# Optimization experiments

Hardware: AMD Instinct MI355X
Metric: run time of the kernel (lower is better)

Reference implementation:

```python
import jax, jax.numpy as jnp
import numpy as np

NUM_HEADS = 16
D_MODEL = 1024
B, T = 2, 2048


def setup_inputs() -> dict:
    key = jax.random.key(0)
    ks = jax.random.split(key, 5)
    s = 1.0 / np.sqrt(D_MODEL)
    return {
        "x": jax.random.normal(ks[0], (B, T, D_MODEL), dtype=jnp.float32),
        "Wq": jax.random.normal(ks[1], (D_MODEL, D_MODEL), dtype=jnp.float32) * s,
        "Wk": jax.random.normal(ks[2], (D_MODEL, D_MODEL), dtype=jnp.float32) * s,
        "Wv": jax.random.normal(ks[3], (D_MODEL, D_MODEL), dtype=jnp.float32) * s,
        "Wo": jax.random.normal(ks[4], (D_MODEL, D_MODEL), dtype=jnp.float32) * s,
    }


def reference(x, Wq, Wk, Wv, Wo):
    # x: [B, T, D]; W*: [D, D] (torch nn.Linear weight layout, y = x @ W.T)
    b, t, d = x.shape
    h = NUM_HEADS
    hd = d // h

    def split_heads(y):
        # [B, T, D] -> [B, H, T, hd]
        return y.reshape(b, t, h, hd).transpose(0, 2, 1, 3)

    q = split_heads(x @ Wq.T)
    k = split_heads(x @ Wk.T)
    v = split_heads(x @ Wv.T)

    # scale uses last dim AFTER head split: 1/sqrt(head_dim)
    scores = jnp.einsum("bhqd,bhkd->bhqk", q, k) / jnp.sqrt(jnp.asarray(hd, x.dtype))
    causal = jnp.tril(jnp.ones((t, t), dtype=bool))  # [T, T]
    scores = jnp.where(causal[None, None], scores, -jnp.inf)
    attn = jax.nn.softmax(scores, axis=-1)  # [B, H, T, T]

    out = jnp.einsum("bhqk,bhkd->bhqd", attn, v)  # [B, H, T, hd]
    out = out.transpose(0, 2, 1, 3).reshape(b, t, d)  # concat heads
    return out @ Wo.T
```

## Files before the change

kernel.cpp:

```cpp
#include <hip/hip_runtime.h>
#include <hip/hip_bf16.h>

#define T_SEQ 2048
#define DM    1024
#define MTOT  4096

typedef short v8s __attribute__((ext_vector_type(8)));
typedef short v4s __attribute__((ext_vector_type(4)));
typedef float v4f __attribute__((ext_vector_type(4)));

__device__ __forceinline__ unsigned short f2bf(float f) {
  union { float f; unsigned int u; } x; x.f = f;
  return (unsigned short)((x.u + (((x.u >> 16) & 1u) + 0x7fffu)) >> 16);
}

__device__ __forceinline__ unsigned int pk2(float a, float b) {
  unsigned int ua = __float_as_uint(a) + 0x8000u;
  unsigned int ub = __float_as_uint(b) + 0x8000u;
  return __builtin_amdgcn_perm(ub, ua, 0x07060302u);
}

__device__ __forceinline__ v8s pack8bf(v4f a, v4f b) {
  union { v8s s; unsigned int u[4]; } o;
  o.u[0] = pk2(a[0], a[1]);
  o.u[1] = pk2(a[2], a[3]);
  o.u[2] = pk2(b[0], b[1]);
  o.u[3] = pk2(b[2], b[3]);
  return o.s;
}

__device__ __forceinline__ float fast_exp2(float x) {
#if __has_builtin(__builtin_amdgcn_exp2f)
  return __builtin_amdgcn_exp2f(x);
#else
  return exp2f(x);
#endif
}

__device__ __forceinline__ void gload16(const void* g, void* lds) {
  __builtin_amdgcn_global_load_lds(
      (const __attribute__((address_space(1))) unsigned int*)g,
      (__attribute__((address_space(3))) unsigned int*)lds, 16, 0, 0);
}

__global__ __launch_bounds__(256) void convert_all(
    const float* __restrict__ x,
    const float* __restrict__ Wq, const float* __restrict__ Wk,
    const float* __restrict__ Wv, const float* __restrict__ Wo,
    unsigned short* __restrict__ xb, unsigned short* __restrict__ wb)
{
  int i = blockIdx.x * 256 + threadIdx.x;
  const float4* src;
  ushort4* dst;
  int idx;
  if (i < (1 << 20)) {
    src = (const float4*)x; dst = (ushort4*)xb; idx = i;
  } else {
    int j = i - (1 << 20);
    int wsel = j >> 18;
    idx = j & ((1 << 18) - 1);
    const float* s = (wsel == 0) ? Wq : (wsel == 1) ? Wk : (wsel == 2) ? Wv : Wo;
    src = (const float4*)s;
    dst = (ushort4*)(wb + (size_t)wsel * DM * DM);
  }
  float4 v = src[idx];
  ushort4 o = { f2bf(v.x), f2bf(v.y), f2bf(v.z), f2bf(v.w) };
  dst[idx] = o;
}

__global__ __launch_bounds__(256) void qkv_fused4(
    const unsigned short* __restrict__ xb,
    const unsigned short* __restrict__ wb,
    unsigned short* __restrict__ Qw, unsigned short* __restrict__ Kw,
    unsigned short* __restrict__ Vtw)
{
  __shared__ unsigned short smem[2][20480];

  const int tid  = threadIdx.x;
  const int wv   = tid >> 6, l = tid & 63;
  const int lrow = l & 15, lq = l >> 4;
  const int wm = wv >> 1;
  const int wn = wv & 1;
  const int srow = l >> 3, sslot = l & 7;
  const int swz  = sslot ^ (srow & 7);
  const int m0 = blockIdx.x * 128, n0 = blockIdx.y * 64;

  v4f acc[3][4][2];
#pragma unroll
  for (int z = 0; z < 3; ++z)
#pragma unroll
    for (int mt = 0; mt < 4; ++mt)
#pragma unroll
      for (int nt = 0; nt < 2; ++nt) acc[z][mt][nt] = (v4f){0.f, 0.f, 0.f, 0.f};

  const size_t aBase = (size_t)(m0 + wv * 32 + srow) * DM + swz * 8;
  const size_t bBase = (size_t)(n0 + wv * 16 + srow) * DM + swz * 8;

#define STG(k0_, buf_) do {                                                   \
    unsigned short* s_ = smem[buf_];                                          \
    _Pragma("unroll")                                                         \
    for (int i_ = 0; i_ < 4; ++i_)                                            \
      gload16(xb + aBase + (size_t)i_ * 8 * DM + (k0_),                       \
              s_ + (wv * 32 + i_ * 8) * 64);                                  \
    _Pragma("unroll")                                                         \
    for (int z_ = 0; z_ < 3; ++z_)                                            \
      _Pragma("unroll")                                                       \
      for (int i_ = 0; i_ < 2; ++i_)                                          \
        gload16(wb + (size_t)z_ * DM * DM + bBase + (size_t)i_ * 8 * DM + (k0_), \
                s_ + 8192 + z_ * 4096 + (wv * 16 + i_ * 8) * 64);             \
  } while (0)

  STG(0, 0);
  __syncthreads();

  int cur = 0;
  for (int k0 = 0; k0 < DM; k0 += 64) {
    if (k0 + 64 < DM) STG(k0 + 64, cur ^ 1);

    const unsigned short* As = smem[cur];
    const unsigned short* Ws = smem[cur] + 8192;
#pragma unroll
    for (int kc = 0; kc < 2; ++kc) {
      const int aslot = ((kc << 2) | lq) ^ (lrow & 7);
      v8s af[4];
#pragma unroll
      for (int mt = 0; mt < 4; ++mt)
        af[mt] = *(const v8s*)&As[(wm * 64 + mt * 16 + lrow) * 64 + aslot * 8];
#pragma unroll
      for (int z = 0; z < 3; ++z) {
        const unsigned short* Bz = Ws + z * 4096;
        v8s bf[2];
#pragma unroll
        for (int nt = 0; nt < 2; ++nt)
          bf[nt] = *(const v8s*)&Bz[(wn * 32 + nt * 16 + lrow) * 64 + aslot * 8];
#pragma unroll
        for (int mt = 0; mt < 4; ++mt)
#pragma unroll
          for (int nt = 0; nt < 2; ++nt)
            acc[z][mt][nt] = __builtin_amdgcn_mfma_f32_16x16x32_bf16(
                af[mt], bf[nt], acc[z][mt][nt], 0, 0, 0);
      }
    }

    if (k0 + 64 < DM) {
      __syncthreads();
      cur ^= 1;
    }
  }
#undef STG

#pragma unroll
  for (int z = 0; z < 2; ++z) {
    unsigned short* Y = z ? Kw : Qw;
#pragma unroll
    for (int mt = 0; mt < 4; ++mt)
#pragma unroll
      for (int nt = 0; nt < 2; ++nt)
#pragma unroll
        for (int r = 0; r < 4; ++r) {
          int row = m0 + wm * 64 + mt * 16 + lq * 4 + r;
          int col = n0 + wn * 32 + nt * 16 + lrow;
          Y[(size_t)row * DM + col] = f2bf(acc[z][mt][nt][r]);
        }
  }

  __syncthreads();
  {
    unsigned short* stg = smem[0];
#pragma unroll
    for (int mt = 0; mt < 4; ++mt)
#pragma unroll
      for (int nt = 0; nt < 2; ++nt)
#pragma unroll
        for (int r = 0; r < 4; ++r) {
          int trow = wm * 64 + mt * 16 + lq * 4 + r;
          int col  = wn * 32 + nt * 16 + lrow;
          int slot = (col >> 3) ^ (trow & 7);
          stg[trow * 64 + slot * 8 + (col & 7)] = f2bf(acc[2][mt][nt][r]);
        }
    __syncthreads();
    {
      const int d = tid & 63;
      const int quarter = tid >> 6;
      const int bb = m0 >> 11;
      const int tblk = (m0 & 2047) >> 7;
      const int h = n0 >> 6;
      const int bh = bb * 16 + h;
      unsigned short* dst = Vtw + (((size_t)bh * 16 + tblk) * 64 + d) * 128;
      const int ch = d >> 3, e7 = d & 7;
#pragma unroll
      for (int jj = 0; jj < 4; ++jj) {
        unsigned short vals[8];
#pragma unroll
        for (int e = 0; e < 8; ++e) {
          int st = quarter * 32 + (e >> 2) * 16 + jj * 4 + (e & 3);
          vals[e] = stg[st * 64 + (ch ^ (st & 7)) * 8 + e7];
        }
        *(v8s*)(dst + (quarter * 4 + jj) * 8) = *(const v8s*)vals;
      }
    }
  }
}

__global__ __launch_bounds__(256) void oproj_gemm2(
    const unsigned short* __restrict__ AO,
    const unsigned short* __restrict__ Wob,
    float* __restrict__ Y)
{
  __shared__ unsigned short smem[12288];
  unsigned short* As = smem;
  unsigned short* Bs = smem + 4096;

  const int tid  = threadIdx.x;
  const int wv   = tid >> 6, l = tid & 63;
  const int lrow = l & 15, lq = l >> 4;
  const int wm = wv >> 1;
  const int wn = wv & 1;
  const int srow = l >> 3, sslot = l & 7;
  const int swz  = sslot ^ (srow & 7);
  const int m0 = blockIdx.x * 64, n0 = blockIdx.y * 128;

  v4f acc[2][4];
#pragma unroll
  for (int mt = 0; mt < 2; ++mt)
#pragma unroll
    for (int nt = 0; nt < 4; ++nt) acc[mt][nt] = (v4f){0.f, 0.f, 0.f, 0.f};

  const size_t aBase = (size_t)(m0 + wv * 16 + srow) * DM + swz * 8;
  const size_t bBase = (size_t)(n0 + wv * 32 + srow) * DM + swz * 8;

  for (int k0 = 0; k0 < DM; k0 += 64) {
    __syncthreads();
#pragma unroll
    for (int i = 0; i < 2; ++i)
      gload16(AO + aBase + (size_t)i * 8 * DM + k0, As + (wv * 16 + i * 8) * 64);
#pragma unroll
    for (int i = 0; i < 4; ++i)
      gload16(Wob + bBase + (size_t)i * 8 * DM + k0, Bs + (wv * 32 + i * 8) * 64);
    __syncthreads();
#pragma unroll
    for (int kc = 0; kc < 2; ++kc) {
      const int aslot = ((kc << 2) | lq) ^ (lrow & 7);
      v8s af[2], bf[4];
#pragma unroll
      for (int mt = 0; mt < 2; ++mt)
        af[mt] = *(const v8s*)&As[(wm * 32 + mt * 16 + lrow) * 64 + aslot * 8];
#pragma unroll
      for (int nt = 0; nt < 4; ++nt)
        bf[nt] = *(const v8s*)&Bs[(wn * 64 + nt * 16 + lrow) * 64 + aslot * 8];
#pragma unroll
      for (int mt = 0; mt < 2; ++mt)
#pragma unroll
        for (int nt = 0; nt < 4; ++nt)
          acc[mt][nt] = __builtin_amdgcn_mfma_f32_16x16x32_bf16(
              af[mt], bf[nt], acc[mt][nt], 0, 0, 0);
    }
  }
#pragma unroll
  for (int mt = 0; mt < 2; ++mt)
#pragma unroll
    for (int nt = 0; nt < 4; ++nt)
#pragma unroll
      for (int r = 0; r < 4; ++r) {
        int row = m0 + wm * 32 + mt * 16 + lq * 4 + r;
        int col = n0 + wn * 64 + nt * 16 + lrow;
        Y[(size_t)row * DM + col] = acc[mt][nt][r];
      }
}

__global__ __launch_bounds__(256) void attn12(
    const unsigned short* __restrict__ Q,
    const unsigned short* __restrict__ K,
    const unsigned short* __restrict__ Vt,
    unsigned short* __restrict__ O)
{
  __shared__ unsigned short Ks[128 * 64];
  __shared__ unsigned short Vts[64 * 128];

  const int tid  = threadIdx.x;
  const int wave = tid >> 6;
  const int lane = tid & 63;
  const int lrow = lane & 15;
  const int lq   = lane >> 4;
  const int gid  = blockIdx.x;
  const int qt   = 31 - (gid >> 5);
  const int bh   = gid & 31;
  const int b = bh >> 4, h = bh & 15;

  union { v8s s; unsigned int u[4]; } ones;
  ones.u[0] = 0x3F803F80u; ones.u[1] = 0x3F803F80u;
  ones.u[2] = 0x3F803F80u; ones.u[3] = 0x3F803F80u;

  const int qrow = qt * 64 + wave * 16 + lrow;
  const unsigned short* qp = Q + ((size_t)(b * T_SEQ + qrow)) * DM + h * 64;
  v8s qf0 = *(const v8s*)(qp + lq * 8);
  v8s qf1 = *(const v8s*)(qp + 32 + lq * 8);

  v4f oacc[4];
#pragma unroll
  for (int dt = 0; dt < 4; ++dt) oacc[dt] = (v4f){0.f, 0.f, 0.f, 0.f};
  v4f sacc = {0.f, 0.f, 0.f, 0.f};

  const int n128 = (qt >> 1) + 1;

  const int kchunk = (lane & 7) ^ ((lane >> 3) & 7);
  const unsigned short* kg =
      K + ((size_t)(b * T_SEQ) + wave * 8 + (lane >> 3)) * DM + h * 64 + kchunk * 8;
  unsigned short* kdst = Ks + (wave * 8) * 64;
  const int vd = wave * 4 + (lane >> 4);
  const int vslot = lane & 15;
  const int vchunk = (vslot & 8) | ((vslot & 7) ^ (vd & 7));
  const unsigned short* vg =
      Vt + ((size_t)bh * 1024 + vd) * 128 + vchunk * 8;
  unsigned short* vdst = Vts + (wave * 4) * 128;

  const int slot0 = lq ^ (lrow & 7);
  const int slot1 = (4 + lq) ^ (lrow & 7);

  for (int tt = 0; tt < n128; ++tt) {
    __syncthreads();
#pragma unroll
    for (int i = 0; i < 4; ++i)
      gload16(kg + ((size_t)tt * 128 + i * 32) * DM, kdst + i * 32 * 64);
#pragma unroll
    for (int i = 0; i < 4; ++i)
      gload16(vg + (size_t)tt * 8192 + i * 2048, vdst + i * 16 * 128);
    __syncthreads();

    const int kb = tt * 128;

    v4f s[8];
#pragma unroll
    for (int nt = 0; nt < 8; ++nt) {
      v4f a = {0.f, 0.f, 0.f, 0.f};
      v8s k0 = *(const v8s*)&Ks[(nt * 16 + lrow) * 64 + slot0 * 8];
      a = __builtin_amdgcn_mfma_f32_16x16x32_bf16(k0, qf0, a, 0, 0, 0);
      v8s k1 = *(const v8s*)&Ks[(nt * 16 + lrow) * 64 + slot1 * 8];
      a = __builtin_amdgcn_mfma_f32_16x16x32_bf16(k1, qf1, a, 0, 0, 0);
      s[nt] = a;
    }

    const bool needmask = (kb + 127 > qt * 64 + wave * 16);
    if (needmask) {
#pragma unroll
      for (int nt = 0; nt < 8; ++nt)
#pragma unroll
        for (int r = 0; r < 4; ++r) {
          float p = fast_exp2(fmaf(s[nt][r], 0.18033688f, -23.0831206f));
          if (kb + nt * 16 + lq * 4 + r > qt * 64 + wave * 16 + lrow) p = 0.f;
          s[nt][r] = p;
        }
    } else {
#pragma unroll
      for (int nt = 0; nt < 8; ++nt)
#pragma unroll
        for (int r = 0; r < 4; ++r)
          s[nt][r] = fast_exp2(fmaf(s[nt][r], 0.18033688f, -23.0831206f));
    }

    v8s pf[4];
#pragma unroll
    for (int kp = 0; kp < 4; ++kp) pf[kp] = pack8bf(s[2 * kp], s[2 * kp + 1]);

#pragma unroll
    for (int kp = 0; kp < 4; ++kp) {
      sacc = __builtin_amdgcn_mfma_f32_16x16x32_bf16(ones.s, pf[kp], sacc, 0, 0, 0);
#pragma unroll
      for (int dt = 0; dt < 4; ++dt) {
        int ch = kp * 4 + lq;
        int slot = (ch & 8) | ((ch & 7) ^ (lrow & 7));
        v8s vv = *(const v8s*)&Vts[(dt * 16 + lrow) * 128 + slot * 8];
        oacc[dt] = __builtin_amdgcn_mfma_f32_16x16x32_bf16(
            vv, pf[kp], oacc[dt], 0, 0, 0);
      }
    }
  }

  const float rinv = 1.0f / sacc[0];

  const int token = qt * 64 + wave * 16 + lrow;
  unsigned short* op = O + ((size_t)(b * T_SEQ + token)) * DM + h * 64;
#pragma unroll
  for (int dt = 0; dt < 4; ++dt) {
    union { v4s s; unsigned int u[2]; } o;
    o.u[0] = pk2(oacc[dt][0] * rinv, oacc[dt][1] * rinv);
    o.u[1] = pk2(oacc[dt][2] * rinv, oacc[dt][3] * rinv);
    *(v4s*)(op + dt * 16 + lq * 4) = o.s;
  }
}

extern "C" void kernel_launch(void* const* d_in, const int* in_sizes, int n_in,
                              void* d_out, int out_size, void* d_ws, size_t ws_size,
                              hipStream_t stream) {
  const float* x  = (const float*)d_in[0];
  const float* Wq = (const float*)d_in[1];
  const float* Wk = (const float*)d_in[2];
  const float* Wv = (const float*)d_in[3];
  const float* Wo = (const float*)d_in[4];
  float* out = (float*)d_out;

  unsigned short* xb  = (unsigned short*)d_ws;
  unsigned short* wb  = xb + (size_t)MTOT * DM;
  unsigned short* Qw  = wb + (size_t)4 * DM * DM;
  unsigned short* Kw  = Qw + (size_t)MTOT * DM;
  unsigned short* Vtw = Kw + (size_t)MTOT * DM;
  unsigned short* AO  = xb;

  convert_all<<<8192, 256, 0, stream>>>(x, Wq, Wk, Wv, Wo, xb, wb);
  qkv_fused4<<<dim3(32, 16), 256, 0, stream>>>(xb, wb, Qw, Kw, Vtw);
  attn12<<<1024, 256, 0, stream>>>(Qw, Kw, Vtw, AO);
  oproj_gemm2<<<dim3(64, 8), 256, 0, stream>>>(AO, wb + (size_t)3 * DM * DM, out);
}
```

Measured before the change: 164.6 us.

## Fuse fp32-to-bf16 conversion into QKV and output-projection GEMM tile loads

Removes the separate convert_all kernel. The QKV and output-projection GEMMs now read fp32 x and the weights directly into registers, round them to bf16 and store them into the swizzled LDS tiles. This saves a launch and the write and re-read of the bf16 copies. In exchange each GEMM block converts its tiles redundantly and reads twice as many bytes from global memory. The asynchronous global_load_lds path is replaced by register staging with explicit LDS writes, which adds register pressure and could cost latency hiding.

```diff
diff --git a/kernel.cpp b/kernel.cpp
--- a/kernel.cpp
+++ b/kernel.cpp
@@ -8,16 +8,28 @@
 typedef short v8s __attribute__((ext_vector_type(8)));
 typedef short v4s __attribute__((ext_vector_type(4)));
 typedef float v4f __attribute__((ext_vector_type(4)));
-
-__device__ __forceinline__ unsigned short f2bf(float f) {
-  union { float f; unsigned int u; } x; x.f = f;
-  return (unsigned short)((x.u + (((x.u >> 16) & 1u) + 0x7fffu)) >> 16);
-}
 
 __device__ __forceinline__ unsigned int pk2(float a, float b) {
   unsigned int ua = __float_as_uint(a) + 0x8000u;
   unsigned int ub = __float_as_uint(b) + 0x8000u;
   return __builtin_amdgcn_perm(ub, ua, 0x07060302u);
+}
+
+__device__ __forceinline__ unsigned int rne2(float a, float b) {
+  unsigned int ua = __float_as_uint(a);
+  ua += ((ua >> 16) & 1u) + 0x7fffu;
+  unsigned int ub = __float_as_uint(b);
+  ub += ((ub >> 16) & 1u) + 0x7fffu;
+  return __builtin_amdgcn_perm(ub, ua, 0x07060302u);
+}
+
+__device__ __forceinline__ v8s pack8f(float4 a, float4 b) {
+  union { v8s s; unsigned int u[4]; } o;
+  o.u[0] = rne2(a.x, a.y);
+  o.u[1] = rne2(a.z, a.w);
+  o.u[2] = rne2(b.x, b.y);
+  o.u[3] = rne2(b.z, b.w);
+  return o.s;
 }
 
 __device__ __forceinline__ v8s pack8bf(v4f a, v4f b) {
@@ -43,34 +55,10 @@
       (__attribute__((address_space(3))) unsigned int*)lds, 16, 0, 0);
 }
 
-__global__ __launch_bounds__(256) void convert_all(
+__global__ __launch_bounds__(256) void qkv_fused5(
     const float* __restrict__ x,
     const float* __restrict__ Wq, const float* __restrict__ Wk,
-    const float* __restrict__ Wv, const float* __restrict__ Wo,
-    unsigned short* __restrict__ xb, unsigned short* __restrict__ wb)
-{
-  int i = blockIdx.x * 256 + threadIdx.x;
-  const float4* src;
-  ushort4* dst;
-  int idx;
-  if (i < (1 << 20)) {
-    src = (const float4*)x; dst = (ushort4*)xb; idx = i;
-  } else {
-    int j = i - (1 << 20);
-    int wsel = j >> 18;
-    idx = j & ((1 << 18) - 1);
-    const float* s = (wsel == 0) ? Wq : (wsel == 1) ? Wk : (wsel == 2) ? Wv : Wo;
-    src = (const float4*)s;
-    dst = (ushort4*)(wb + (size_t)wsel * DM * DM);
-  }
-  float4 v = src[idx];
-  ushort4 o = { f2bf(v.x), f2bf(v.y), f2bf(v.z), f2bf(v.w) };
-  dst[idx] = o;
-}
-
-__global__ __launch_bounds__(256) void qkv_fused4(
-    const unsigned short* __restrict__ xb,
-    const unsigned short* __restrict__ wb,
+    const float* __restrict__ Wv,
     unsigned short* __restrict__ Qw, unsigned short* __restrict__ Kw,
     unsigned short* __restrict__ Vtw)
 {
@@ -93,29 +81,52 @@
 #pragma unroll
       for (int nt = 0; nt < 2; ++nt) acc[z][mt][nt] = (v4f){0.f, 0.f, 0.f, 0.f};
 
-  const size_t aBase = (size_t)(m0 + wv * 32 + srow) * DM + swz * 8;
-  const size_t bBase = (size_t)(n0 + wv * 16 + srow) * DM + swz * 8;
-
-#define STG(k0_, buf_) do {                                                   \
+  const float* axp = x + (size_t)(m0 + wv * 32 + srow) * DM + swz * 8;
+  const float* wp0 = Wq + (size_t)(n0 + wv * 16 + srow) * DM + swz * 8;
+  const float* wp1 = Wk + (size_t)(n0 + wv * 16 + srow) * DM + swz * 8;
+  const float* wp2 = Wv + (size_t)(n0 + wv * 16 + srow) * DM + swz * 8;
+
+  float4 ra[4][2];
+  float4 rw[3][2][2];
+
+#define STG_LOAD(k0_) do {                                                    \
+    _Pragma("unroll")                                                         \
+    for (int i_ = 0; i_ < 4; ++i_) {                                          \
+      ra[i_][0] = *(const float4*)(axp + (size_t)i_ * 8 * DM + (k0_));        \
+      ra[i_][1] = *(const float4*)(axp + (size_t)i_ * 8 * DM + (k0_) + 4);    \
+    }                                                                         \
+    _Pragma("unroll")                                                         \
+    for (int i_ = 0; i_ < 2; ++i_) {                                          \
+      rw[0][i_][0] = *(const float4*)(wp0 + (size_t)i_ * 8 * DM + (k0_));     \
+      rw[0][i_][1] = *(const float4*)(wp0 + (size_t)i_ * 8 * DM + (k0_) + 4); \
+      rw[1][i_][0] = *(const float4*)(wp1 + (size_t)i_ * 8 * DM + (k0_));     \
+      rw[1][i_][1] = *(const float4*)(wp1 + (size_t)i_ * 8 * DM + (k0_) + 4); \
+      rw[2][i_][0] = *(const float4*)(wp2 + (size_t)i_ * 8 * DM + (k0_));     \
+      rw[2][i_][1] = *(const float4*)(wp2 + (size_t)i_ * 8 * DM + (k0_) + 4); \
+    }                                                                         \
+  } while (0)
+
+#define STG_WRITE(buf_) do {                                                  \
     unsigned short* s_ = smem[buf_];                                          \
     _Pragma("unroll")                                                         \
     for (int i_ = 0; i_ < 4; ++i_)                                            \
-      gload16(xb + aBase + (size_t)i_ * 8 * DM + (k0_),                       \
-              s_ + (wv * 32 + i_ * 8) * 64);                                  \
+      *(v8s*)&s_[(wv * 32 + i_ * 8 + srow) * 64 + sslot * 8] =                \
+          pack8f(ra[i_][0], ra[i_][1]);                                       \
     _Pragma("unroll")                                                         \
     for (int z_ = 0; z_ < 3; ++z_)                                            \
       _Pragma("unroll")                                                       \
       for (int i_ = 0; i_ < 2; ++i_)                                          \
-        gload16(wb + (size_t)z_ * DM * DM + bBase + (size_t)i_ * 8 * DM + (k0_), \
-                s_ + 8192 + z_ * 4096 + (wv * 16 + i_ * 8) * 64);             \
+        *(v8s*)&s_[8192 + z_ * 4096 + (wv * 16 + i_ * 8 + srow) * 64 + sslot * 8] = \
+            pack8f(rw[z_][i_][0], rw[z_][i_][1]);                             \
   } while (0)
 
-  STG(0, 0);
+  STG_LOAD(0);
+  STG_WRITE(0);
   __syncthreads();
 
   int cur = 0;
   for (int k0 = 0; k0 < DM; k0 += 64) {
-    if (k0 + 64 < DM) STG(k0 + 64, cur ^ 1);
+    if (k0 + 64 < DM) STG_LOAD(k0 + 64);
 
     const unsigned short* As = smem[cur];
     const unsigned short* Ws = smem[cur] + 8192;
@@ -143,11 +154,13 @@
     }
 
     if (k0 + 64 < DM) {
+      STG_WRITE(cur ^ 1);
       __syncthreads();
       cur ^= 1;
     }
   }
-#undef STG
+#undef STG_LOAD
+#undef STG_WRITE
 
 #pragma unroll
   for (int z = 0; z < 2; ++z) {
@@ -160,7 +173,8 @@
         for (int r = 0; r < 4; ++r) {
           int row = m0 + wm * 64 + mt * 16 + lq * 4 + r;
           int col = n0 + wn * 32 + nt * 16 + lrow;
-          Y[(size_t)row * DM + col] = f2bf(acc[z][mt][nt][r]);
+          unsigned int p = rne2(acc[z][mt][nt][r], 0.f);
+          Y[(size_t)row * DM + col] = (unsigned short)p;
         }
   }
 
@@ -176,7 +190,8 @@
           int trow = wm * 64 + mt * 16 + lq * 4 + r;
           int col  = wn * 32 + nt * 16 + lrow;
           int slot = (col >> 3) ^ (trow & 7);
-          stg[trow * 64 + slot * 8 + (col & 7)] = f2bf(acc[2][mt][nt][r]);
+          stg[trow * 64 + slot * 8 + (col & 7)] =
+              (unsigned short)rne2(acc[2][mt][nt][r], 0.f);
         }
     __syncthreads();
     {
@@ -202,9 +217,9 @@
   }
 }
 
-__global__ __launch_bounds__(256) void oproj_gemm2(
+__global__ __launch_bounds__(256) void oproj_gemm3(
     const unsigned short* __restrict__ AO,
-    const unsigned short* __restrict__ Wob,
+    const float* __restrict__ Wo,
     float* __restrict__ Y)
 {
   __shared__ unsigned short smem[12288];
@@ -227,16 +242,23 @@
     for (int nt = 0; nt < 4; ++nt) acc[mt][nt] = (v4f){0.f, 0.f, 0.f, 0.f};
 
   const size_t aBase = (size_t)(m0 + wv * 16 + srow) * DM + swz * 8;
-  const size_t bBase = (size_t)(n0 + wv * 32 + srow) * DM + swz * 8;
+  const float* wop = Wo + (size_t)(n0 + wv * 32 + srow) * DM + swz * 8;
 
   for (int k0 = 0; k0 < DM; k0 += 64) {
     __syncthreads();
+    float4 rb[4][2];
+#pragma unroll
+    for (int i = 0; i < 4; ++i) {
+      rb[i][0] = *(const float4*)(wop + (size_t)i * 8 * DM + k0);
+      rb[i][1] = *(const float4*)(wop + (size_t)i * 8 * DM + k0 + 4);
+    }
 #pragma unroll
     for (int i = 0; i < 2; ++i)
       gload16(AO + aBase + (size_t)i * 8 * DM + k0, As + (wv * 16 + i * 8) * 64);
 #pragma unroll
     for (int i = 0; i < 4; ++i)
-      gload16(Wob + bBase + (size_t)i * 8 * DM + k0, Bs + (wv * 32 + i * 8) * 64);
+      *(v8s*)&Bs[(wv * 32 + i * 8 + srow) * 64 + sslot * 8] =
+          pack8f(rb[i][0], rb[i][1]);
     __syncthreads();
 #pragma unroll
     for (int kc = 0; kc < 2; ++kc) {
@@ -399,15 +421,12 @@
   const float* Wo = (const float*)d_in[4];
   float* out = (float*)d_out;
 
-  unsigned short* xb  = (unsigned short*)d_ws;
-  unsigned short* wb  = xb + (size_t)MTOT * DM;
-  unsigned short* Qw  = wb + (size_t)4 * DM * DM;
+  unsigned short* Qw  = (unsigned short*)d_ws;
   unsigned short* Kw  = Qw + (size_t)MTOT * DM;
   unsigned short* Vtw = Kw + (size_t)MTOT * DM;
-  unsigned short* AO  = xb;
-
-  convert_all<<<8192, 256, 0, stream>>>(x, Wq, Wk, Wv, Wo, xb, wb);
-  qkv_fused4<<<dim3(32, 16), 256, 0, stream>>>(xb, wb, Qw, Kw, Vtw);
+  unsigned short* AO  = Vtw + (size_t)MTOT * DM;
+
+  qkv_fused5<<<dim3(32, 16), 256, 0, stream>>>(x, Wq, Wk, Wv, Qw, Kw, Vtw);
   attn12<<<1024, 256, 0, stream>>>(Qw, Kw, Vtw, AO);
-  oproj_gemm2<<<dim3(64, 8), 256, 0, stream>>>(AO, wb + (size_t)3 * DM * DM, out);
-}
+  oproj_gemm3<<<dim3(64, 8), 256, 0, stream>>>(AO, Wo, out);
+}
```

New measurement: 205.6 us. 1.25x slower.
